# Performance work log

Measured on AMD Instinct MI355X. Metric: run time of the kernel, lower is better.

Reference implementation:

```python
import jax, jax.numpy as jnp
import numpy as np

COMMITMENT_COST = 1.0


def setup_inputs() -> dict:
    key = jax.random.key(0)
    k1, k2 = jax.random.split(key)
    B, D, H, W = 32, 256, 32, 32
    K = 1024
    z = jax.random.normal(k1, (B, D, H, W), dtype=jnp.float32)
    # torch init: uniform(-1/K, 1/K)
    codebook = jax.random.uniform(k2, (K, D), dtype=jnp.float32,
                                  minval=-1.0 / K, maxval=1.0 / K)
    return {"z": z, "codebook": codebook}


def reference(z, codebook):
    B, D, H, W = z.shape
    # (B, D, H, W) -> (B, H, W, D) -> (N, D)
    zp = jnp.transpose(z, (0, 2, 3, 1))
    zf = zp.reshape(-1, D)
    # squared euclidean distances (N, K): ||z||^2 + ||e||^2 - 2 z.e
    d = (jnp.sum(zf * zf, axis=1, keepdims=True)
         + jnp.sum(codebook * codebook, axis=1)
         - 2.0 * jnp.matmul(zf, codebook.T))
    idx = jnp.argmin(d, axis=1)                    # (N,)
    zq = codebook[idx].reshape(B, H, W, D)         # gather
    vq_loss = jnp.mean((jax.lax.stop_gradient(zq) - zp) ** 2)
    commitment_loss = jnp.mean((zq - jax.lax.stop_gradient(zp)) ** 2)
    loss = vq_loss + COMMITMENT_COST * commitment_loss
    # straight-through estimator
    zq_st = zp + jax.lax.stop_gradient(zq - zp)
    zq_out = jnp.transpose(zq_st, (0, 3, 1, 2))    # back to (B, D, H, W)
    indices = idx.reshape(B, H, W)
    return zq_out, indices, loss
```

## Files before the change

### kernel.cpp

```cpp
#include <hip/hip_runtime.h>

#define NPOS 32768
#define DDIM 256
#define KCODE 1024
#define HW 1024
#define BSTRIDE (256*1024)
#define OUT0_SIZE 8388608
#define OUT1_SIZE 32768

#define WS_ET     0
#define WS_ZN2    262144
#define WS_EN     327680
#define WS_PACKED 328704

typedef float f32x8 __attribute__((ext_vector_type(8)));

__device__ __forceinline__ const float* uniform_ptr(const float* p) {
    unsigned long long u = (unsigned long long)(uintptr_t)p;
    unsigned lo = __builtin_amdgcn_readfirstlane((unsigned)u);
    unsigned hi = __builtin_amdgcn_readfirstlane((unsigned)(u >> 32));
    return (const float*)(((unsigned long long)hi << 32) | lo);
}

__global__ void vq_prep(const float* __restrict__ z,
                        const float* __restrict__ cb,
                        float* __restrict__ ws_f,
                        unsigned long long* __restrict__ packed,
                        float* __restrict__ loss_slot) {
    __shared__ float tile[64][65];
    int bx = blockIdx.x;
    int t  = threadIdx.x;

    if (bx < 256) {
        int p = t >> 1, h = t & 1;
        int n = bx * 128 + p;
        int b = n >> 10, hw = n & 1023;
        const float* base = z + (size_t)b * BSTRIDE + hw + (size_t)(h * 128) * HW;
        float r[8];
        #pragma unroll
        for (int j = 0; j < 8; ++j) {
            float v = base[(size_t)j * HW];
            r[j] = __fmul_rn(v, v);
        }
        #pragma unroll
        for (int i = 8; i < 128; i += 8) {
            #pragma unroll
            for (int j = 0; j < 8; ++j) {
                float v = base[(size_t)(i + j) * HW];
                r[j] = __fadd_rn(r[j], __fmul_rn(v, v));
            }
        }
        float half_s = __fadd_rn(
            __fadd_rn(__fadd_rn(r[0], r[1]), __fadd_rn(r[2], r[3])),
            __fadd_rn(__fadd_rn(r[4], r[5]), __fadd_rn(r[6], r[7])));
        ws_f[WS_ZN2 + 2 * n + h] = half_s;
        if (h == 0) packed[n] = 0xFFFFFFFFFFFFFFFFull;
        if (bx == 0 && t == 0) *loss_slot = 0.0f;
    } else if (bx < 260) {
        int k = (bx - 256) * 256 + t;
        const float* row = cb + (size_t)k * DDIM;
        float half_s[2];
        #pragma unroll
        for (int h = 0; h < 2; ++h) {
            const float* p2 = row + h * 128;
            float r[8];
            #pragma unroll
            for (int j = 0; j < 8; ++j) r[j] = __fmul_rn(p2[j], p2[j]);
            #pragma unroll
            for (int i = 8; i < 128; i += 8) {
                #pragma unroll
                for (int j = 0; j < 8; ++j)
                    r[j] = __fadd_rn(r[j], __fmul_rn(p2[i + j], p2[i + j]));
            }
            half_s[h] = __fadd_rn(
                __fadd_rn(__fadd_rn(r[0], r[1]), __fadd_rn(r[2], r[3])),
                __fadd_rn(__fadd_rn(r[4], r[5]), __fadd_rn(r[6], r[7])));
        }
        ws_f[WS_EN + k] = __fadd_rn(half_s[0], half_s[1]);
    } else {
        int bt = bx - 260;
        int k0 = (bt & 15) * 64;
        int d0 = (bt >> 4) * 64;
        float* et = ws_f + WS_ET;
        #pragma unroll
        for (int p = 0; p < 4; ++p) {
            int r  = p * 16 + (t >> 4);
            int c4 = (t & 15) * 4;
            float4 v = *reinterpret_cast<const float4*>(
                cb + (size_t)(k0 + r) * DDIM + d0 + c4);
            tile[r][c4] = v.x; tile[r][c4+1] = v.y;
            tile[r][c4+2] = v.z; tile[r][c4+3] = v.w;
        }
        __syncthreads();
        #pragma unroll
        for (int s = 0; s < 16; ++s) {
            int dd = s * 4 + (t >> 6);
            int kk = t & 63;
            et[(size_t)(d0 + dd) * KCODE + k0 + kk] = tile[kk][dd];
        }
    }
}

#define BM 64
#define BN 512
#define BK 16
#define BSKEW(k) ((k) + ((k) >> 3))

__launch_bounds__(512, 4)
__global__ void vq_argmin(const float* __restrict__ z,
                          const float* __restrict__ ws_f,
                          unsigned long long* __restrict__ packed) {
    __shared__ float Bs[BK][576];

    const float* ET  = ws_f + WS_ET;
    const float* zn2 = ws_f + WS_ZN2;
    const float* enW = ws_f + WS_EN;

    int t  = threadIdx.x;
    int l  = t & 63;
    int w_ = __builtin_amdgcn_readfirstlane(t >> 6);
    int bc = blockIdx.x & 1;
    int bm = blockIdx.x >> 1;
    int kc = bc * BN;
    int n0 = bm * BM;
    int b  = n0 >> 10, hw0 = n0 & 1023;
    const __attribute__((address_space(4))) f32x8* zc =
        (const __attribute__((address_space(4))) f32x8*)(uintptr_t)
            uniform_ptr(z + (size_t)b * BSTRIDE + hw0 + 8 * w_);

    float acc[8][8];
    #pragma unroll
    for (int j = 0; j < 8; ++j)
        #pragma unroll
        for (int c = 0; c < 8; ++c) acc[j][c] = 0.0f;

    for (int d0 = 0; d0 < DDIM; d0 += BK) {
        __syncthreads();
        #pragma unroll
        for (int i = 0; i < 4; ++i) {
            int q = t + i * 512;
            int dk = q >> 7, m = q & 127;
            float4 v = *reinterpret_cast<const float4*>(
                ET + (size_t)(d0 + dk) * KCODE + kc + 4 * m);
            int ph = BSKEW(4 * m);
            *reinterpret_cast<float4*>(&Bs[dk][ph]) = v;
        }
        __syncthreads();

        #pragma unroll
        for (int dh = 0; dh < BK; dh += 4) {
            f32x8 aw[4];
            #pragma unroll
            for (int dd = 0; dd < 4; ++dd)
                aw[dd] = zc[(size_t)(d0 + dh + dd) * (HW / 8)];
            float4 b0[4], b1[4];
            #pragma unroll
            for (int dd = 0; dd < 4; ++dd) {
                b0[dd] = *reinterpret_cast<const float4*>(&Bs[dh + dd][9 * l]);
                b1[dd] = *reinterpret_cast<const float4*>(&Bs[dh + dd][9 * l + 4]);
            }
            #pragma unroll
            for (int dd = 0; dd < 4; ++dd) {
                float bb[8] = {b0[dd].x, b0[dd].y, b0[dd].z, b0[dd].w,
                               b1[dd].x, b1[dd].y, b1[dd].z, b1[dd].w};
                #pragma unroll
                for (int j = 0; j < 8; ++j) {
                    float aj = aw[dd][j];
                    #pragma unroll
                    for (int c = 0; c < 8; ++c)
                        acc[j][c] = fmaf(aj, bb[c], acc[j][c]);
                }
            }
        }
    }

    float znr[8];
    #pragma unroll
    for (int j = 0; j < 8; ++j) {
        int n = n0 + 8 * w_ + j;
        znr[j] = __fadd_rn(zn2[2 * n], zn2[2 * n + 1]);
    }
    float4 e0 = *reinterpret_cast<const float4*>(enW + kc + 8 * l);
    float4 e1 = *reinterpret_cast<const float4*>(enW + kc + 8 * l + 4);
    float en8[8] = {e0.x, e0.y, e0.z, e0.w, e1.x, e1.y, e1.z, e1.w};

    float m1[8];
    int   i1[8];
    #pragma unroll
    for (int j = 0; j < 8; ++j) { m1[j] = 1e30f; i1[j] = 0; }
    #pragma unroll
    for (int c = 0; c < 8; ++c) {
        int k = kc + 8 * l + c;
        float ek = en8[c];
        #pragma unroll
        for (int j = 0; j < 8; ++j) {
            float t1 = __fadd_rn(znr[j], ek);
            float d  = __fsub_rn(t1, __fmul_rn(2.0f, acc[j][c]));
            if (d < m1[j]) { m1[j] = d; i1[j] = k; }
        }
    }

    #pragma unroll
    for (int j = 0; j < 8; ++j) {
        float a1v = m1[j];
        int   ii  = i1[j];
        #pragma unroll
        for (int off = 1; off < 64; off <<= 1) {
            float o1 = __shfl_xor(a1v, off, 64);
            int   oi = __shfl_xor(ii, off, 64);
            if (o1 < a1v || (o1 == a1v && oi < ii)) { a1v = o1; ii = oi; }
        }
        if (l == 0) {
            unsigned long long key =
                ((unsigned long long)__float_as_uint(a1v) << 32) |
                (unsigned long long)(unsigned)ii;
            atomicMin(&packed[n0 + 8 * w_ + j], key);
        }
    }
}

__global__ void vq_gather(const float* __restrict__ z,
                          const float* __restrict__ cb,
                          const unsigned long long* __restrict__ packed,
                          float* __restrict__ out,
                          float* __restrict__ loss) {
    int t  = threadIdx.x;
    int p  = t & 63, dc = t >> 6;
    int n  = blockIdx.x * 64 + p;
    int b  = n >> 10, hw = n & 1023;
    int k  = (int)(unsigned)(packed[n] & 0xFFFFFFFFull);
    size_t off = (size_t)b * BSTRIDE + hw + (size_t)(dc * 64) * HW;
    const float* e  = cb + (size_t)k * DDIM + dc * 64;
    const float* zp = z + off;
    float* op = out + off;
    float s = 0.0f;
    #pragma unroll 4
    for (int d4 = 0; d4 < 16; ++d4) {
        float4 ev = *reinterpret_cast<const float4*>(e + 4 * d4);
        float evs[4] = {ev.x, ev.y, ev.z, ev.w};
        #pragma unroll
        for (int q = 0; q < 4; ++q) {
            int d = 4 * d4 + q;
            float zv = zp[(size_t)d * HW];
            op[(size_t)d * HW] = evs[q];
            float df = evs[q] - zv;
            s = fmaf(df, df, s);
        }
    }
    if (dc == 0) out[OUT0_SIZE + n] = (float)k;

    #pragma unroll
    for (int o = 32; o > 0; o >>= 1) s += __shfl_down(s, o);
    __shared__ float red[4];
    int lane = t & 63, w = t >> 6;
    if (lane == 0) red[w] = s;
    __syncthreads();
    if (t == 0) {
        float tot = (red[0] + red[1] + red[2] + red[3]) * (2.0f / 8388608.0f);
        atomicAdd(loss, tot);
    }
}

extern "C" void kernel_launch(void* const* d_in, const int* in_sizes, int n_in,
                              void* d_out, int out_size, void* d_ws, size_t ws_size,
                              hipStream_t stream) {
    const float* z  = (const float*)d_in[0];
    const float* cb = (const float*)d_in[1];
    float* out  = (float*)d_out;
    float* ws_f = (float*)d_ws;
    unsigned long long* packed =
        (unsigned long long*)(ws_f + WS_PACKED);
    float* loss = out + OUT0_SIZE + OUT1_SIZE;

    vq_prep<<<324, 256, 0, stream>>>(z, cb, ws_f, packed, loss);
    vq_argmin<<<(NPOS / BM) * (KCODE / BN), 512, 0, stream>>>(z, ws_f, packed);
    vq_gather<<<NPOS / 64, 256, 0, stream>>>(z, cb, packed, out, loss);
}
```

Before: 355.3 us.

## Stage z tile in LDS and stream codebook directly from global

The argmin GEMM swaps which operand is staged: the 16x64 z tile now goes into shared memory, and each thread reads its 8 codebook columns straight from global memory with one-step register prefetch. The old scalar-load path for z is dropped. Blocks shrink to 256 threads covering 64 positions by 256 codes, giving four code chunks per position group and twice as many blocks. The cost is more global traffic for the codebook, no LDS reuse of those loads, and twice as many atomicMin merges per position.

```diff
diff --git a/kernel.cpp b/kernel.cpp
--- a/kernel.cpp
+++ b/kernel.cpp
@@ -12,15 +12,6 @@
 #define WS_ZN2    262144
 #define WS_EN     327680
 #define WS_PACKED 328704
-
-typedef float f32x8 __attribute__((ext_vector_type(8)));
-
-__device__ __forceinline__ const float* uniform_ptr(const float* p) {
-    unsigned long long u = (unsigned long long)(uintptr_t)p;
-    unsigned lo = __builtin_amdgcn_readfirstlane((unsigned)u);
-    unsigned hi = __builtin_amdgcn_readfirstlane((unsigned)(u >> 32));
-    return (const float*)(((unsigned long long)hi << 32) | lo);
-}
 
 __global__ void vq_prep(const float* __restrict__ z,
                         const float* __restrict__ cb,
@@ -102,31 +93,29 @@
 }
 
 #define BM 64
-#define BN 512
+#define BN 256
 #define BK 16
-#define BSKEW(k) ((k) + ((k) >> 3))
-
-__launch_bounds__(512, 4)
+
+__launch_bounds__(256, 4)
 __global__ void vq_argmin(const float* __restrict__ z,
                           const float* __restrict__ ws_f,
                           unsigned long long* __restrict__ packed) {
-    __shared__ float Bs[BK][576];
+    __shared__ float As[BK][64];
 
     const float* ET  = ws_f + WS_ET;
     const float* zn2 = ws_f + WS_ZN2;
     const float* enW = ws_f + WS_EN;
 
     int t  = threadIdx.x;
-    int l  = t & 63;
-    int w_ = __builtin_amdgcn_readfirstlane(t >> 6);
-    int bc = blockIdx.x & 1;
-    int bm = blockIdx.x >> 1;
+    int tx = t & 31;
+    int ty = t >> 5;
+    int bc = blockIdx.x & 3;
+    int bm = blockIdx.x >> 2;
     int kc = bc * BN;
     int n0 = bm * BM;
     int b  = n0 >> 10, hw0 = n0 & 1023;
-    const __attribute__((address_space(4))) f32x8* zc =
-        (const __attribute__((address_space(4))) f32x8*)(uintptr_t)
-            uniform_ptr(z + (size_t)b * BSTRIDE + hw0 + 8 * w_);
+    const float* zb = z + (size_t)b * BSTRIDE + hw0;
+    const float* bp = ET + kc + 8 * tx;
 
     float acc[8][8];
     #pragma unroll
@@ -136,52 +125,46 @@
 
     for (int d0 = 0; d0 < DDIM; d0 += BK) {
         __syncthreads();
-        #pragma unroll
-        for (int i = 0; i < 4; ++i) {
-            int q = t + i * 512;
-            int dk = q >> 7, m = q & 127;
+        {
+            int dk = t >> 4, p4 = (t & 15) << 2;
             float4 v = *reinterpret_cast<const float4*>(
-                ET + (size_t)(d0 + dk) * KCODE + kc + 4 * m);
-            int ph = BSKEW(4 * m);
-            *reinterpret_cast<float4*>(&Bs[dk][ph]) = v;
+                zb + (size_t)(d0 + dk) * HW + p4);
+            As[dk][p4] = v.x; As[dk][p4+1] = v.y;
+            As[dk][p4+2] = v.z; As[dk][p4+3] = v.w;
         }
         __syncthreads();
 
-        #pragma unroll
-        for (int dh = 0; dh < BK; dh += 4) {
-            f32x8 aw[4];
-            #pragma unroll
-            for (int dd = 0; dd < 4; ++dd)
-                aw[dd] = zc[(size_t)(d0 + dh + dd) * (HW / 8)];
-            float4 b0[4], b1[4];
-            #pragma unroll
-            for (int dd = 0; dd < 4; ++dd) {
-                b0[dd] = *reinterpret_cast<const float4*>(&Bs[dh + dd][9 * l]);
-                b1[dd] = *reinterpret_cast<const float4*>(&Bs[dh + dd][9 * l + 4]);
+        float4 nb0 = *reinterpret_cast<const float4*>(bp + (size_t)d0 * KCODE);
+        float4 nb1 = *reinterpret_cast<const float4*>(bp + (size_t)d0 * KCODE + 4);
+        #pragma unroll
+        for (int dk = 0; dk < BK; ++dk) {
+            float4 b0 = nb0, b1 = nb1;
+            if (dk < BK - 1) {
+                nb0 = *reinterpret_cast<const float4*>(
+                    bp + (size_t)(d0 + dk + 1) * KCODE);
+                nb1 = *reinterpret_cast<const float4*>(
+                    bp + (size_t)(d0 + dk + 1) * KCODE + 4);
             }
-            #pragma unroll
-            for (int dd = 0; dd < 4; ++dd) {
-                float bb[8] = {b0[dd].x, b0[dd].y, b0[dd].z, b0[dd].w,
-                               b1[dd].x, b1[dd].y, b1[dd].z, b1[dd].w};
+            float4 a0 = *reinterpret_cast<const float4*>(&As[dk][ty * 8]);
+            float4 a1 = *reinterpret_cast<const float4*>(&As[dk][ty * 8 + 4]);
+            float a[8]  = {a0.x, a0.y, a0.z, a0.w, a1.x, a1.y, a1.z, a1.w};
+            float bb[8] = {b0.x, b0.y, b0.z, b0.w, b1.x, b1.y, b1.z, b1.w};
+            #pragma unroll
+            for (int j = 0; j < 8; ++j)
                 #pragma unroll
-                for (int j = 0; j < 8; ++j) {
-                    float aj = aw[dd][j];
-                    #pragma unroll
-                    for (int c = 0; c < 8; ++c)
-                        acc[j][c] = fmaf(aj, bb[c], acc[j][c]);
-                }
-            }
+                for (int c = 0; c < 8; ++c)
+                    acc[j][c] = fmaf(a[j], bb[c], acc[j][c]);
         }
     }
 
     float znr[8];
     #pragma unroll
     for (int j = 0; j < 8; ++j) {
-        int n = n0 + 8 * w_ + j;
+        int n = n0 + ty * 8 + j;
         znr[j] = __fadd_rn(zn2[2 * n], zn2[2 * n + 1]);
     }
-    float4 e0 = *reinterpret_cast<const float4*>(enW + kc + 8 * l);
-    float4 e1 = *reinterpret_cast<const float4*>(enW + kc + 8 * l + 4);
+    float4 e0 = *reinterpret_cast<const float4*>(enW + kc + 8 * tx);
+    float4 e1 = *reinterpret_cast<const float4*>(enW + kc + 8 * tx + 4);
     float en8[8] = {e0.x, e0.y, e0.z, e0.w, e1.x, e1.y, e1.z, e1.w};
 
     float m1[8];
@@ -190,7 +173,7 @@
     for (int j = 0; j < 8; ++j) { m1[j] = 1e30f; i1[j] = 0; }
     #pragma unroll
     for (int c = 0; c < 8; ++c) {
-        int k = kc + 8 * l + c;
+        int k = kc + 8 * tx + c;
         float ek = en8[c];
         #pragma unroll
         for (int j = 0; j < 8; ++j) {
@@ -205,16 +188,16 @@
         float a1v = m1[j];
         int   ii  = i1[j];
         #pragma unroll
-        for (int off = 1; off < 64; off <<= 1) {
-            float o1 = __shfl_xor(a1v, off, 64);
-            int   oi = __shfl_xor(ii, off, 64);
+        for (int off = 1; off < 32; off <<= 1) {
+            float o1 = __shfl_xor(a1v, off, 32);
+            int   oi = __shfl_xor(ii, off, 32);
             if (o1 < a1v || (o1 == a1v && oi < ii)) { a1v = o1; ii = oi; }
         }
-        if (l == 0) {
+        if (tx == 0) {
             unsigned long long key =
                 ((unsigned long long)__float_as_uint(a1v) << 32) |
                 (unsigned long long)(unsigned)ii;
-            atomicMin(&packed[n0 + 8 * w_ + j], key);
+            atomicMin(&packed[n0 + ty * 8 + j], key);
         }
     }
 }
@@ -273,6 +256,6 @@
     float* loss = out + OUT0_SIZE + OUT1_SIZE;
 
     vq_prep<<<324, 256, 0, stream>>>(z, cb, ws_f, packed, loss);
-    vq_argmin<<<(NPOS / BM) * (KCODE / BN), 512, 0, stream>>>(z, ws_f, packed);
+    vq_argmin<<<(NPOS / BM) * (KCODE / BN), 256, 0, stream>>>(z, ws_f, packed);
     vq_gather<<<NPOS / 64, 256, 0, stream>>>(z, cb, packed, out, loss);
 }
```

Measured after the change: 401.4 us. +13.0%, slower.
